# Kernel optimization log

Hardware: AMD Instinct MI355X
Metric: run time of the kernel (lower is better)

## Reference

```python
import jax, jax.numpy as jnp
import numpy as np

NEG_SLOPE = 0.01  # torch nn.LeakyReLU default

B, N, IN_F, OUT_F, HEADS = 4, 2048, 512, 512, 8
D = OUT_F // HEADS  # 64


def setup_inputs() -> dict:
    key = jax.random.key(0)
    ks = jax.random.split(key, 4)
    X = jax.random.normal(ks[0], (B, N, IN_F), dtype=jnp.float32)
    W_v = jax.random.normal(ks[1], (IN_F, D), dtype=jnp.float32) * (IN_F ** -0.5)
    b_v = jnp.zeros((D,), dtype=jnp.float32)
    W_q = jax.random.normal(ks[2], (D, HEADS), dtype=jnp.float32) * (D ** -0.5)
    b_q = jnp.zeros((HEADS,), dtype=jnp.float32)
    W_k = jax.random.normal(ks[3], (D, HEADS), dtype=jnp.float32) * (D ** -0.5)
    b_k = jnp.zeros((HEADS,), dtype=jnp.float32)
    return {"X": X, "W_v": W_v, "b_v": b_v, "W_q": W_q, "b_q": b_q, "W_k": W_k, "b_k": b_k}


def reference(X, W_v, b_v, W_q, b_q, W_k, b_k):
    # V: (B, N, D)
    V = X @ W_v + b_v
    # per-node, per-head scalar scores: (B, N, H) -> (B, H, N)
    Q = jnp.swapaxes(V @ W_q + b_q, 1, 2)
    K = jnp.swapaxes(V @ W_k + b_k, 1, 2)
    # A[b,h,i,j] = leaky_relu(Q[b,h,j] + K[b,h,i])  (broadcast outer-sum)
    A = jax.nn.leaky_relu(Q[:, :, None, :] + K[:, :, :, None], negative_slope=NEG_SLOPE)
    A = jax.nn.softmax(A, axis=-1)  # dropout = identity in eval mode
    # H[b,i,h,f] = sum_j A[b,h,i,j] V[b,j,f]
    H = jnp.einsum('bhij,bjf->bihf', A, V)
    return H.reshape(H.shape[0], H.shape[1], -1)  # (B, N, H*D)
```

## Files before the change

### kernel.cpp

```cpp
#include <hip/hip_runtime.h>

#define BB   4
#define NN   2048
#define INF  512
#define HH   8
#define DD   64
#define BH   (BB*HH)
#define NCK  16
#define CKS  128
#define KSP  8


__global__ __launch_bounds__(256) void k_vpart(
    const float* __restrict__ X, const float* __restrict__ Wv,
    float* __restrict__ Vpart)
{
  const int t   = threadIdx.x;
  const int d   = t & 63;
  const int wid = __builtin_amdgcn_readfirstlane(blockIdx.x * 4 + (t >> 6));
  const int rg  = wid >> 3;
  const int ks  = wid & 7;
  const int k0  = ks * 64;
  float wreg[64];
  const float* wp = Wv + (size_t)k0 * DD + d;
  #pragma unroll
  for (int kk = 0; kk < 64; kk++) wreg[kk] = wp[(size_t)kk * DD];
  const float* xp = X + (size_t)(rg * 16) * INF + k0;
  float* vp = Vpart + ((size_t)ks * (BB*NN) + (size_t)rg * 16) * DD + d;
  for (int r = 0; r < 16; r++) {
    float a0 = 0.f, a1 = 0.f, a2 = 0.f, a3 = 0.f;
    #pragma unroll
    for (int kk = 0; kk < 64; kk += 4) {
      a0 += xp[kk+0] * wreg[kk+0];
      a1 += xp[kk+1] * wreg[kk+1];
      a2 += xp[kk+2] * wreg[kk+2];
      a3 += xp[kk+3] * wreg[kk+3];
    }
    vp[(size_t)r * DD] = (a0 + a1) + (a2 + a3);
    xp += INF;
  }
}

__global__ __launch_bounds__(256) void k_vred(
    const float* __restrict__ Vpart, const float* __restrict__ bv,
    const float* __restrict__ Wq, const float* __restrict__ bq,
    const float* __restrict__ Wk, const float* __restrict__ bk,
    float* __restrict__ V, float* __restrict__ qsg, float* __restrict__ ksg)
{
  __shared__ float Vs[16][DD + 1];
  const int t  = threadIdx.x;
  const size_t e0 = ((size_t)blockIdx.x * 256 + t) * 4;
  const size_t STR = (size_t)BB * NN * DD;
  float4 a = *(const float4*)(Vpart + e0);
  #pragma unroll
  for (int p = 1; p < KSP; p++) {
    const float4 b = *(const float4*)(Vpart + (size_t)p * STR + e0);
    a.x += b.x;  a.y += b.y;  a.z += b.z;  a.w += b.w;
  }
  const float4 bb = *(const float4*)(bv + (e0 & 63));
  a.x += bb.x;  a.y += bb.y;  a.z += bb.z;  a.w += bb.w;
  *(float4*)(V + e0) = a;
  const int lrow = t >> 4;
  const int lcol = (t * 4) & 63;
  Vs[lrow][lcol]   = a.x;  Vs[lrow][lcol+1] = a.y;
  Vs[lrow][lcol+2] = a.z;  Vs[lrow][lcol+3] = a.w;
  __syncthreads();
  const int row = t >> 4;
  const int h   = t & 7;
  const bool isK = (t & 8) != 0;
  const float* W = isK ? Wk : Wq;
  float s = isK ? bk[h] : bq[h];
  #pragma unroll 8
  for (int dd = 0; dd < DD; dd++) s += Vs[row][dd] * W[dd*HH + h];
  const int grow = blockIdx.x * 16 + row;
  const int b = grow >> 11, n = grow & (NN - 1);
  (isK ? ksg : qsg)[(b*HH + h) * NN + n] = s;
}

__global__ __launch_bounds__(1024) void k_sort(
    float* __restrict__ q, unsigned short* __restrict__ idxg)
{
  __shared__ float key[NN];
  __shared__ int   idx[NN];
  const int t  = threadIdx.x;
  const int bh = blockIdx.x;
  key[t]        = q[bh*NN + t];        idx[t]        = t;
  key[t + 1024] = q[bh*NN + t + 1024]; idx[t + 1024] = t + 1024;
  __syncthreads();

#define CEX_STAGE(size, stride)                                         \
  {                                                                     \
    const int i = ((t & ~((stride) - 1)) << 1) | (t & ((stride) - 1));  \
    const int j = i + (stride);                                         \
    const bool up = ((i & (size)) == 0);                                \
    const float a = key[i], b = key[j];                                 \
    if (up ? (a > b) : (a < b)) {                                       \
      key[i] = b; key[j] = a;                                           \
      const int tmp = idx[i]; idx[i] = idx[j]; idx[j] = tmp;            \
    }                                                                   \
  }

  for (int size = 2; size <= 128; size <<= 1)
    for (int stride = size >> 1; stride > 0; stride >>= 1)
      CEX_STAGE(size, stride)
  __syncthreads();
  for (int size = 256; size <= 2048; size <<= 1) {
    for (int stride = size >> 1; stride >= 128; stride >>= 1) {
      CEX_STAGE(size, stride)
      __syncthreads();
    }
    for (int stride = 64; stride > 0; stride >>= 1)
      CEX_STAGE(size, stride)
    __syncthreads();
  }
#undef CEX_STAGE

  q[bh*NN + t]        = key[t];
  q[bh*NN + t + 1024] = key[t + 1024];
  idxg[bh*NN + t]        = (unsigned short)idx[t];
  idxg[bh*NN + t + 1024] = (unsigned short)idx[t + 1024];
}

__global__ __launch_bounds__(256) void k_scan(
    const float* __restrict__ sq, const unsigned short* __restrict__ idxg,
    const float* __restrict__ V,
    float* __restrict__ P1, float* __restrict__ P2,
    float* __restrict__ l1, float* __restrict__ l2,
    float* __restrict__ S1g, float* __restrict__ S2g,
    float* __restrict__ SL1, float* __restrict__ SL2)
{
  __shared__ float ss1[4][64], ss2[4][64], sl1[4], sl2[4];
  const int t  = threadIdx.x;
  const int bh = blockIdx.x >> 4;
  const int ck = blockIdx.x & 15;
  const int d  = t & 63, g = t >> 6;
  const int r0 = ck*CKS + g*32;
  const float* Vb  = V + (size_t)(bh >> 3) * NN * DD;
  const float* sqb = sq + bh*NN;
  const unsigned short* ib = idxg + bh*NN;
  float a1 = 0.f, a2 = 0.f, s1 = 0.f, s2 = 0.f;
  #pragma unroll 8
  for (int rr = 0; rr < 32; rr++) {
    const int r = r0 + rr;
    const float qv = sqb[r];
    const float e1 = __expf(qv), e2 = __expf(0.01f*qv);
    const float v  = Vb[(size_t)ib[r]*DD + d];
    a1 += e1*v;  a2 += e2*v;  s1 += e1;  s2 += e2;
  }
  ss1[g][d] = a1;  ss2[g][d] = a2;
  if (d == 0) { sl1[g] = s1;  sl2[g] = s2; }
  __syncthreads();
  float o1 = 0.f, o2 = 0.f, lo1 = 0.f, lo2 = 0.f;
  for (int gg = 0; gg < g; gg++) { o1 += ss1[gg][d]; o2 += ss2[gg][d]; lo1 += sl1[gg]; lo2 += sl2[gg]; }
  if (g == 0) {
    S1g[(bh*NCK + ck)*64 + d] = ss1[0][d]+ss1[1][d]+ss1[2][d]+ss1[3][d];
    S2g[(bh*NCK + ck)*64 + d] = ss2[0][d]+ss2[1][d]+ss2[2][d]+ss2[3][d];
    if (d == 0) {
      SL1[bh*NCK + ck] = sl1[0]+sl1[1]+sl1[2]+sl1[3];
      SL2[bh*NCK + ck] = sl2[0]+sl2[1]+sl2[2]+sl2[3];
    }
  }
  a1 = o1; a2 = o2; s1 = lo1; s2 = lo2;
  float* P1b = P1 + (size_t)bh*NN*DD;
  float* P2b = P2 + (size_t)bh*NN*DD;
  #pragma unroll 8
  for (int rr = 0; rr < 32; rr++) {
    const int r = r0 + rr;
    const float qv = sqb[r];
    const float e1 = __expf(qv), e2 = __expf(0.01f*qv);
    const float v  = Vb[(size_t)ib[r]*DD + d];
    P1b[(size_t)r*DD + d] = a1;
    P2b[(size_t)r*DD + d] = a2;
    if (d == 0) { l1[bh*NN + r] = s1;  l2[bh*NN + r] = s2; }
    a1 += e1*v;  a2 += e2*v;  s1 += e1;  s2 += e2;
  }
}

__global__ __launch_bounds__(256) void k_off(
    const float* __restrict__ S1g, const float* __restrict__ S2g,
    const float* __restrict__ SL1, const float* __restrict__ SL2,
    float* __restrict__ Off1, float* __restrict__ Off2,
    float* __restrict__ Loff1, float* __restrict__ Loff2)
{
  const int bh = blockIdx.x;
  const int t  = threadIdx.x;
  if (t < 128) {
    const int d = t & 63;
    const bool h2 = t >= 64;
    const float* S = h2 ? S2g : S1g;
    float* O = h2 ? Off2 : Off1;
    double a = 0.0;
    for (int ck = 0; ck < NCK; ck++) {
      O[((size_t)bh*(NCK+1) + ck)*64 + d] = (float)a;
      a += (double)S[((size_t)bh*NCK + ck)*64 + d];
    }
    O[((size_t)bh*(NCK+1) + NCK)*64 + d] = (float)a;
  } else if (t == 128 || t == 129) {
    const bool h2 = (t == 129);
    const float* S = h2 ? SL2 : SL1;
    float* O = h2 ? Loff2 : Loff1;
    double a = 0.0;
    for (int ck = 0; ck < NCK; ck++) { O[bh*(NCK+1) + ck] = (float)a; a += (double)S[bh*NCK + ck]; }
    O[bh*(NCK+1) + NCK] = (float)a;
  }
}

__global__ __launch_bounds__(256) void k_out(
    const float* __restrict__ sq, const float* __restrict__ ksg,
    const float* __restrict__ P1, const float* __restrict__ P2,
    const float* __restrict__ Off1, const float* __restrict__ Off2,
    const float* __restrict__ l1, const float* __restrict__ l2,
    const float* __restrict__ Loff1, const float* __restrict__ Loff2,
    float* __restrict__ out)
{
  const int t  = threadIdx.x;
  const int bh = blockIdx.x >> 9;
  const int i  = ((blockIdx.x & 511) << 2) + (t >> 6);
  const int d  = t & 63;
  const int b  = bh >> 3, h = bh & 7;
  const float kv = ksg[bh*NN + i];
  const float tt = -kv;
  const float* s = sq + bh*NN;
  const unsigned long long m1 = __ballot(s[d*32 + 31] <= tt);
  const int c1 = __popcll(m1);
  int pos;
  if (c1 == 64) pos = NN;
  else {
    const int bs = c1 << 5;
    const unsigned long long m2 = __ballot(s[bs + (d & 31)] <= tt);
    pos = bs + (__popcll(m2) >> 1);
  }
  const float ek  = __expf(kv);
  const float ek2 = __expf(0.01f * kv);
  const size_t base = (size_t)bh * NN * DD;
  const float T1  = Off1[((size_t)bh*(NCK+1) + NCK)*64 + d];
  const float Lt1 = Loff1[bh*(NCK+1) + NCK];
  float p1v, p2v, q1v, q2v;
  if (pos < NN) {
    const int ch = pos >> 7;
    p1v = P1[base + (size_t)pos*DD + d] + Off1[((size_t)bh*(NCK+1) + ch)*64 + d];
    p2v = P2[base + (size_t)pos*DD + d] + Off2[((size_t)bh*(NCK+1) + ch)*64 + d];
    q1v = l1[bh*NN + pos] + Loff1[bh*(NCK+1) + ch];
    q2v = l2[bh*NN + pos] + Loff2[bh*(NCK+1) + ch];
  } else {
    p1v = T1;   p2v = Off2[((size_t)bh*(NCK+1) + NCK)*64 + d];
    q1v = Lt1;  q2v = Loff2[bh*(NCK+1) + NCK];
  }
  const float num = ek * (T1 - p1v)  + ek2 * p2v;
  const float den = ek * (Lt1 - q1v) + ek2 * q2v;
  out[((size_t)(b*NN + i)) * (HH*DD) + h*DD + d] = num / den;
}

extern "C" void kernel_launch(void* const* d_in, const int* in_sizes, int n_in,
                              void* d_out, int out_size, void* d_ws, size_t ws_size,
                              hipStream_t stream)
{
  (void)in_sizes; (void)n_in; (void)out_size; (void)ws_size;
  const float* X  = (const float*)d_in[0];
  const float* Wv = (const float*)d_in[1];
  const float* bv = (const float*)d_in[2];
  const float* Wq = (const float*)d_in[3];
  const float* bq = (const float*)d_in[4];
  const float* Wk = (const float*)d_in[5];
  const float* bk = (const float*)d_in[6];
  float* out = (float*)d_out;

  float* w = (float*)d_ws;
  float* V     = w;  w += (size_t)BB*NN*DD;
  float* qsg   = w;  w += BH*NN;
  float* ksg   = w;  w += BH*NN;
  float* l1    = w;  w += BH*NN;
  float* l2    = w;  w += BH*NN;
  unsigned short* idxg = (unsigned short*)w;  w += BH*NN/2;
  float* Off1  = w;  w += BH*(NCK+1)*DD;
  float* Off2  = w;  w += BH*(NCK+1)*DD;
  float* Loff1 = w;  w += BH*(NCK+1);
  float* Loff2 = w;  w += BH*(NCK+1);
  float* P1    = w;  w += (size_t)BH*NN*DD;
  float* P2    = w;  w += (size_t)BH*NN*DD;

  float* Vpart = P1;

  float* S1g = out;
  float* S2g = S1g + BH*NCK*DD;
  float* SL1 = S2g + BH*NCK*DD;
  float* SL2 = SL1 + BH*NCK;

  k_vpart<<<1024, 256, 0, stream>>>(X, Wv, Vpart);
  k_vred <<<512, 256, 0, stream>>>(Vpart, bv, Wq, bq, Wk, bk, V, qsg, ksg);
  k_sort <<<BH, 1024, 0, stream>>>(qsg, idxg);
  k_scan <<<BH*NCK, 256, 0, stream>>>(qsg, idxg, V, P1, P2, l1, l2, S1g, S2g, SL1, SL2);
  k_off  <<<BH, 256, 0, stream>>>(S1g, S2g, SL1, SL2, Off1, Off2, Loff1, Loff2);
  k_out  <<<BH*512, 256, 0, stream>>>(qsg, ksg, P1, P2, Off1, Off2, l1, l2, Loff1, Loff2, out);
}
```

Measured before the change: 157.4 us.

## Register-tile V projection, stash gathered V in LDS, batch rows in output kernel

The V projection kernel now stages a 64x64 weight slice in shared memory and has each thread compute an 8x8 register tile from float4 loads of X, replacing the per-thread 64-register weight vector design. The scan kernel caches the gathered V rows in LDS during its first pass so the second pass does not repeat the indirect global gather. The output kernel handles four query rows per wavefront, reusing the probe load and launching four times fewer blocks. These aim to cut redundant global loads and launch overhead, at the cost of more registers and LDS per block.

```diff
diff --git a/kernel.cpp b/kernel.cpp
--- a/kernel.cpp
+++ b/kernel.cpp
@@ -11,33 +11,57 @@
 #define KSP  8
 
 
-__global__ __launch_bounds__(256) void k_vpart(
+__global__ __launch_bounds__(128) void k_v(
     const float* __restrict__ X, const float* __restrict__ Wv,
     float* __restrict__ Vpart)
 {
-  const int t   = threadIdx.x;
-  const int d   = t & 63;
-  const int wid = __builtin_amdgcn_readfirstlane(blockIdx.x * 4 + (t >> 6));
-  const int rg  = wid >> 3;
-  const int ks  = wid & 7;
-  const int k0  = ks * 64;
-  float wreg[64];
-  const float* wp = Wv + (size_t)k0 * DD + d;
-  #pragma unroll
-  for (int kk = 0; kk < 64; kk++) wreg[kk] = wp[(size_t)kk * DD];
-  const float* xp = X + (size_t)(rg * 16) * INF + k0;
-  float* vp = Vpart + ((size_t)ks * (BB*NN) + (size_t)rg * 16) * DD + d;
-  for (int r = 0; r < 16; r++) {
-    float a0 = 0.f, a1 = 0.f, a2 = 0.f, a3 = 0.f;
+  __shared__ float Ws[64][68];
+  const int t  = threadIdx.x;
+  const int tc = t & 7;
+  const int tr = t >> 3;
+  const int rg = blockIdx.x >> 3;
+  const int ks = blockIdx.x & 7;
+  const int r0 = rg * 128;
+  const int k0 = ks * 64;
+
+  #pragma unroll
+  for (int i = 0; i < 8; i++) {
+    const int e4 = t + i * 128;
+    const int k  = e4 >> 4;
+    const int n4 = (e4 & 15) * 4;
+    *(float4*)(&Ws[k][n4]) = *(const float4*)(Wv + (size_t)(k0 + k) * DD + n4);
+  }
+  __syncthreads();
+
+  float acc[8][8] = {{0.f}};
+  const float* xbase = X + (size_t)(r0 + tr * 8) * INF + k0;
+  for (int kk = 0; kk < 64; kk += 4) {
+    float4 xv[8];
     #pragma unroll
-    for (int kk = 0; kk < 64; kk += 4) {
-      a0 += xp[kk+0] * wreg[kk+0];
-      a1 += xp[kk+1] * wreg[kk+1];
-      a2 += xp[kk+2] * wreg[kk+2];
-      a3 += xp[kk+3] * wreg[kk+3];
-    }
-    vp[(size_t)r * DD] = (a0 + a1) + (a2 + a3);
-    xp += INF;
+    for (int r = 0; r < 8; r++)
+      xv[r] = *(const float4*)(xbase + (size_t)r * INF + kk);
+    #pragma unroll
+    for (int j = 0; j < 4; j++) {
+      const float4 wa = *(const float4*)(&Ws[kk + j][tc * 8]);
+      const float4 wb = *(const float4*)(&Ws[kk + j][tc * 8 + 4]);
+      #pragma unroll
+      for (int r = 0; r < 8; r++) {
+        const float x = (j == 0) ? xv[r].x : (j == 1) ? xv[r].y : (j == 2) ? xv[r].z : xv[r].w;
+        acc[r][0] += x * wa.x;  acc[r][1] += x * wa.y;
+        acc[r][2] += x * wa.z;  acc[r][3] += x * wa.w;
+        acc[r][4] += x * wb.x;  acc[r][5] += x * wb.y;
+        acc[r][6] += x * wb.z;  acc[r][7] += x * wb.w;
+      }
+    }
+  }
+  float* vp = Vpart + ((size_t)ks * (BB*NN) + r0 + tr * 8) * DD + tc * 8;
+  #pragma unroll
+  for (int r = 0; r < 8; r++) {
+    float4 oa, ob;
+    oa.x = acc[r][0]; oa.y = acc[r][1]; oa.z = acc[r][2]; oa.w = acc[r][3];
+    ob.x = acc[r][4]; ob.y = acc[r][5]; ob.z = acc[r][6]; ob.w = acc[r][7];
+    *(float4*)(vp + (size_t)r * DD)     = oa;
+    *(float4*)(vp + (size_t)r * DD + 4) = ob;
   }
 }
 
@@ -129,6 +153,7 @@
     float* __restrict__ S1g, float* __restrict__ S2g,
     float* __restrict__ SL1, float* __restrict__ SL2)
 {
+  __shared__ float vstash[4][32][DD];
   __shared__ float ss1[4][64], ss2[4][64], sl1[4], sl2[4];
   const int t  = threadIdx.x;
   const int bh = blockIdx.x >> 4;
@@ -145,6 +170,7 @@
     const float qv = sqb[r];
     const float e1 = __expf(qv), e2 = __expf(0.01f*qv);
     const float v  = Vb[(size_t)ib[r]*DD + d];
+    vstash[g][rr][d] = v;
     a1 += e1*v;  a2 += e2*v;  s1 += e1;  s2 += e2;
   }
   ss1[g][d] = a1;  ss2[g][d] = a2;
@@ -168,7 +194,7 @@
     const int r = r0 + rr;
     const float qv = sqb[r];
     const float e1 = __expf(qv), e2 = __expf(0.01f*qv);
-    const float v  = Vb[(size_t)ib[r]*DD + d];
+    const float v  = vstash[g][rr][d];
     P1b[(size_t)r*DD + d] = a1;
     P2b[(size_t)r*DD + d] = a2;
     if (d == 0) { l1[bh*NN + r] = s1;  l2[bh*NN + r] = s2; }
@@ -213,42 +239,52 @@
     const float* __restrict__ Loff1, const float* __restrict__ Loff2,
     float* __restrict__ out)
 {
-  const int t  = threadIdx.x;
-  const int bh = blockIdx.x >> 9;
-  const int i  = ((blockIdx.x & 511) << 2) + (t >> 6);
-  const int d  = t & 63;
-  const int b  = bh >> 3, h = bh & 7;
-  const float kv = ksg[bh*NN + i];
-  const float tt = -kv;
+  const int t   = threadIdx.x;
+  const int bh  = blockIdx.x >> 7;
+  const int loc = blockIdx.x & 127;
+  const int w   = t >> 6;
+  const int d   = t & 63;
+  const int i0  = loc*16 + w*4;
+  const int b   = bh >> 3, h = bh & 7;
   const float* s = sq + bh*NN;
-  const unsigned long long m1 = __ballot(s[d*32 + 31] <= tt);
-  const int c1 = __popcll(m1);
-  int pos;
-  if (c1 == 64) pos = NN;
-  else {
-    const int bs = c1 << 5;
-    const unsigned long long m2 = __ballot(s[bs + (d & 31)] <= tt);
-    pos = bs + (__popcll(m2) >> 1);
-  }
-  const float ek  = __expf(kv);
-  const float ek2 = __expf(0.01f * kv);
-  const size_t base = (size_t)bh * NN * DD;
+  const float probe = s[d*32 + 31];
   const float T1  = Off1[((size_t)bh*(NCK+1) + NCK)*64 + d];
   const float Lt1 = Loff1[bh*(NCK+1) + NCK];
-  float p1v, p2v, q1v, q2v;
-  if (pos < NN) {
-    const int ch = pos >> 7;
-    p1v = P1[base + (size_t)pos*DD + d] + Off1[((size_t)bh*(NCK+1) + ch)*64 + d];
-    p2v = P2[base + (size_t)pos*DD + d] + Off2[((size_t)bh*(NCK+1) + ch)*64 + d];
-    q1v = l1[bh*NN + pos] + Loff1[bh*(NCK+1) + ch];
-    q2v = l2[bh*NN + pos] + Loff2[bh*(NCK+1) + ch];
-  } else {
-    p1v = T1;   p2v = Off2[((size_t)bh*(NCK+1) + NCK)*64 + d];
-    q1v = Lt1;  q2v = Loff2[bh*(NCK+1) + NCK];
-  }
-  const float num = ek * (T1 - p1v)  + ek2 * p2v;
-  const float den = ek * (Lt1 - q1v) + ek2 * q2v;
-  out[((size_t)(b*NN + i)) * (HH*DD) + h*DD + d] = num / den;
+  const size_t base = (size_t)bh * NN * DD;
+
+  float kv[4], tt[4];
+  int pos[4];
+  #pragma unroll
+  for (int u = 0; u < 4; u++) { kv[u] = ksg[bh*NN + i0 + u];  tt[u] = -kv[u]; }
+  #pragma unroll
+  for (int u = 0; u < 4; u++) {
+    const unsigned long long m1 = __ballot(probe <= tt[u]);
+    const int c1 = __popcll(m1);
+    if (c1 == 64) pos[u] = NN;
+    else {
+      const unsigned long long m2 = __ballot(s[c1*32 + (d & 31)] <= tt[u]);
+      pos[u] = c1*32 + (__popcll(m2) >> 1);
+    }
+  }
+  #pragma unroll
+  for (int u = 0; u < 4; u++) {
+    const float ek  = __expf(kv[u]);
+    const float ek2 = __expf(0.01f * kv[u]);
+    float p1v, p2v, q1v, q2v;
+    if (pos[u] < NN) {
+      const int ch = pos[u] >> 7;
+      p1v = P1[base + (size_t)pos[u]*DD + d] + Off1[((size_t)bh*(NCK+1) + ch)*64 + d];
+      p2v = P2[base + (size_t)pos[u]*DD + d] + Off2[((size_t)bh*(NCK+1) + ch)*64 + d];
+      q1v = l1[bh*NN + pos[u]] + Loff1[bh*(NCK+1) + ch];
+      q2v = l2[bh*NN + pos[u]] + Loff2[bh*(NCK+1) + ch];
+    } else {
+      p1v = T1;   p2v = Off2[((size_t)bh*(NCK+1) + NCK)*64 + d];
+      q1v = Lt1;  q2v = Loff2[bh*(NCK+1) + NCK];
+    }
+    const float num = ek * (T1 - p1v)  + ek2 * p2v;
+    const float den = ek * (Lt1 - q1v) + ek2 * q2v;
+    out[((size_t)(b*NN + i0 + u)) * (HH*DD) + h*DD + d] = num / den;
+  }
 }
 
 extern "C" void kernel_launch(void* const* d_in, const int* in_sizes, int n_in,
@@ -286,10 +322,10 @@
   float* SL1 = S2g + BH*NCK*DD;
   float* SL2 = SL1 + BH*NCK;
 
-  k_vpart<<<1024, 256, 0, stream>>>(X, Wv, Vpart);
+  k_v    <<<512, 128, 0, stream>>>(X, Wv, Vpart);
   k_vred <<<512, 256, 0, stream>>>(Vpart, bv, Wq, bq, Wk, bk, V, qsg, ksg);
   k_sort <<<BH, 1024, 0, stream>>>(qsg, idxg);
   k_scan <<<BH*NCK, 256, 0, stream>>>(qsg, idxg, V, P1, P2, l1, l2, S1g, S2g, SL1, SL2);
   k_off  <<<BH, 256, 0, stream>>>(S1g, S2g, SL1, SL2, Off1, Off2, Loff1, Loff2);
-  k_out  <<<BH*512, 256, 0, stream>>>(qsg, ksg, P1, P2, Off1, Off2, l1, l2, Loff1, Loff2, out);
-}
+  k_out  <<<BH*128, 256, 0, stream>>>(qsg, ksg, P1, P2, Off1, Off2, l1, l2, Loff1, Loff2, out);
+}
```

Result: faster. 145.8 us (-7.4%).
